# Kernel tuning notes

Hardware: AMD Instinct MI355X
Metric: run time of the kernel (lower is better)

## Reference

```python
import jax, jax.numpy as jnp
import numpy as np

L, H, DK = 4, 8, 64
NEG = -1e9
PAD = -9999.0


def _ln(z, g, b, eps=1e-6):
    # LayerNormalization: uses unbiased std (torch default) and divides by (std + eps)
    m = jnp.mean(z, axis=-1, keepdims=True)
    s = jnp.std(z, axis=-1, keepdims=True, ddof=1)
    return g * (z - m) / (s + eps) + b


def _mha(q_in, kv_in, w, bw, pw, pb, lnp, mask):
    B, Sq, D = q_in.shape
    q = (q_in @ w[0] + bw[0]).reshape(B, Sq, H, DK).transpose(0, 2, 1, 3)
    k = (kv_in @ w[1] + bw[1]).reshape(B, -1, H, DK).transpose(0, 2, 1, 3)
    v = (kv_in @ w[2] + bw[2]).reshape(B, -1, H, DK).transpose(0, 2, 1, 3)
    scores = jnp.einsum('bhqd,bhkd->bhqk', q, k) * (1.0 / np.sqrt(DK))
    if mask is not None:
        scores = jnp.where(mask[:, None, :, :], NEG, scores)
    attn = jax.nn.softmax(scores, axis=-1)
    ctx = jnp.einsum('bhqk,bhkd->bhqd', attn, v).transpose(0, 2, 1, 3).reshape(B, Sq, H * DK)
    return _ln(q_in + ctx @ pw + pb, lnp[0], lnp[1])


def _ffn(x, w1, b1, w2, b2, lnp):
    # kernel-1 conv1d == pointwise linear; w1:[d_ff,d_model], w2:[d_model,d_ff]
    h = jax.nn.relu(jnp.einsum('bsd,fd->bsf', x, w1) + b1)
    o = jnp.einsum('bsf,df->bsd', h, w2) + b2
    return _ln(x + o, lnp[0], lnp[1])


def _forward(enc_inputs, dec_inputs, emb_w, emb_b, pos_table,
             e_qkv_w, e_qkv_b, e_pw, e_pb, e_ln1, e_w1, e_b1, e_w2, e_b2, e_ln2,
             ds_qkv_w, ds_qkv_b, ds_pw, ds_pb, d_ln1,
             dc_qkv_w, dc_qkv_b, dc_pw, dc_pb, d_ln2,
             d_w1, d_b1, d_w2, d_b2, d_ln3):
    B, Se, F = enc_inputs.shape
    Sd = dec_inputs.shape[1]
    # ConvEmbeddingLayer: kernel-1 conv producing (d_model - n_features) channels, concat with raw inputs
    enc = jnp.concatenate([enc_inputs, jnp.einsum('bsf,of->bso', enc_inputs, emb_w) + emb_b], axis=-1)
    dec = jnp.concatenate([dec_inputs, jnp.einsum('bsf,of->bso', dec_inputs, emb_w) + emb_b], axis=-1)
    # PosEncoding with full lengths -> rows 1..S of the padded table
    enc = enc + pos_table[1:Se + 1]
    dec = dec + pos_table[1:Sd + 1]
    # masks per get_attn_pad_mask / get_attn_subsequent_mask
    enc_pad = jnp.sum(enc_inputs, axis=-1) <= PAD  # [B,Se]
    dec_pad = jnp.sum(dec_inputs, axis=-1) <= PAD  # [B,Sd]
    enc_mask = jnp.broadcast_to(enc_pad[:, None, :], (B, Se, Se))
    causal = jnp.triu(jnp.ones((Sd, Sd), dtype=bool), 1)
    dec_self_mask = jnp.broadcast_to(dec_pad[:, None, :], (B, Sd, Sd)) | causal
    cross_mask = jnp.broadcast_to(enc_pad[:, None, :], (B, Sd, Se))
    for i in range(L):
        enc = _mha(enc, enc, e_qkv_w[i], e_qkv_b[i], e_pw[i], e_pb[i], e_ln1[i], enc_mask)
        enc = _ffn(enc, e_w1[i], e_b1[i], e_w2[i], e_b2[i], e_ln2[i])
    for i in range(L):
        dec = _mha(dec, dec, ds_qkv_w[i], ds_qkv_b[i], ds_pw[i], ds_pb[i], d_ln1[i], dec_self_mask)
        dec = _mha(dec, enc, dc_qkv_w[i], dc_qkv_b[i], dc_pw[i], dc_pb[i], d_ln2[i], cross_mask)
        dec = _ffn(dec, d_w1[i], d_b1[i], d_w2[i], d_b2[i], d_ln3[i])
    return dec


def setup_inputs() -> dict:
    B, Se, Sd, F, Dm, Dff = 8, 512, 512, 32, 512, 2048
    key = jax.random.key(0)
    ks = iter(jax.random.split(key, 32))
    s = 0.02

    def n(shape, sc=s):
        return jax.random.normal(next(ks), shape, jnp.float32) * sc

    # sinusoidal PosEncoding table with leading pad row
    pos = np.arange(Se, dtype=np.float64)[:, None]
    j = np.arange(Dm)[None, :]
    ang = pos / np.power(10000.0, 2.0 * (j // 2) / Dm)
    ang[:, 0::2] = np.sin(ang[:, 0::2])
    ang[:, 1::2] = np.cos(ang[:, 1::2])
    pos_table = jnp.asarray(np.concatenate([np.zeros((1, Dm)), ang]).astype(np.float32))

    ln = jnp.broadcast_to(jnp.stack([jnp.ones(Dm), jnp.zeros(Dm)]), (L, 2, Dm)).astype(jnp.float32) + 0.0
    return {
        'enc_inputs': jax.random.normal(next(ks), (B, Se, F), jnp.float32),
        'dec_inputs': jax.random.normal(next(ks), (B, Sd, F), jnp.float32),
        'emb_w': n((Dm - F, F)), 'emb_b': jnp.zeros(Dm - F, jnp.float32),
        'pos_table': pos_table,
        'e_qkv_w': n((L, 3, Dm, H * DK)), 'e_qkv_b': jnp.zeros((L, 3, H * DK), jnp.float32),
        'e_pw': n((L, H * DK, Dm)), 'e_pb': jnp.zeros((L, Dm), jnp.float32), 'e_ln1': ln,
        'e_w1': n((L, Dff, Dm)), 'e_b1': jnp.zeros((L, Dff), jnp.float32),
        'e_w2': n((L, Dm, Dff)), 'e_b2': jnp.zeros((L, Dm), jnp.float32), 'e_ln2': ln,
        'ds_qkv_w': n((L, 3, Dm, H * DK)), 'ds_qkv_b': jnp.zeros((L, 3, H * DK), jnp.float32),
        'ds_pw': n((L, H * DK, Dm)), 'ds_pb': jnp.zeros((L, Dm), jnp.float32), 'd_ln1': ln,
        'dc_qkv_w': n((L, 3, Dm, H * DK)), 'dc_qkv_b': jnp.zeros((L, 3, H * DK), jnp.float32),
        'dc_pw': n((L, H * DK, Dm)), 'dc_pb': jnp.zeros((L, Dm), jnp.float32), 'd_ln2': ln,
        'd_w1': n((L, Dff, Dm)), 'd_b1': jnp.zeros((L, Dff), jnp.float32),
        'd_w2': n((L, Dm, Dff)), 'd_b2': jnp.zeros((L, Dm), jnp.float32), 'd_ln3': ln,
    }


def reference(enc_inputs, dec_inputs, emb_w, emb_b, pos_table,
              e_qkv_w, e_qkv_b, e_pw, e_pb, e_ln1, e_w1, e_b1, e_w2, e_b2, e_ln2,
              ds_qkv_w, ds_qkv_b, ds_pw, ds_pb, d_ln1,
              dc_qkv_w, dc_qkv_b, dc_pw, dc_pb, d_ln2,
              d_w1, d_b1, d_w2, d_b2, d_ln3):
    return _forward(enc_inputs, dec_inputs, emb_w, emb_b, pos_table,
                    e_qkv_w, e_qkv_b, e_pw, e_pb, e_ln1, e_w1, e_b1, e_w2, e_b2, e_ln2,
                    ds_qkv_w, ds_qkv_b, ds_pw, ds_pb, d_ln1,
                    dc_qkv_w, dc_qkv_b, dc_pw, dc_pb, d_ln2,
                    d_w1, d_b1, d_w2, d_b2, d_ln3)
```

## Files before the change

kernel.cpp:

```cpp
#include <hip/hip_runtime.h>
#include <cstdint>
#include <cstddef>

typedef unsigned short u16;
typedef __bf16 bf16x8 __attribute__((ext_vector_type(8)));
typedef float f32x4 __attribute__((ext_vector_type(4)));

constexpr int Bz = 8, Sq = 512, Hh = 8, DKd = 64, Dm = 512, Dff = 2048, NL = 4;
constexpr int TOK = Bz * Sq;
constexpr size_t MAT = (size_t)512 * 512;
constexpr size_t EL  = (size_t)TOK * Dm;
constexpr size_t WFT = (size_t)Dff * Dm;

__device__ __forceinline__ float bf2f(u16 u) {
  union { uint32_t i; float f; } v; v.i = (uint32_t)u << 16; return v.f;
}
__device__ __forceinline__ u16 f2bf(float f) {
  union { float f; uint32_t i; } v; v.f = f;
  uint32_t i = v.i;
  i += 0x7fffu + ((i >> 16) & 1u);
  return (u16)(i >> 16);
}

__device__ __forceinline__ void gload16(const u16* g, u16* l) {
  __builtin_amdgcn_global_load_lds(
      (const __attribute__((address_space(1))) unsigned int*)g,
      (__attribute__((address_space(3))) unsigned int*)l, 16, 0, 0);
}

template<int BM, int BN>
__global__ __launch_bounds__(256)
void gemm_tile(const u16* __restrict__ A, const u16* __restrict__ Bt,
               const float* __restrict__ bias, u16* __restrict__ C,
               int K, int lda, long long sA, int ldb, long long sB,
               int ldc, long long sC, int cmode, int relu, int colofs,
               const u16* A2, int xsplit)
{
  constexpr int HM = BM / 2, HN = BN / 2, MI = HM / 16, NI = HN / 16;
  __shared__ __align__(16) u16 As[BM * 64];
  __shared__ __align__(16) u16 Bs[BN * 64];
  const int bz = blockIdx.z;
  const u16* Abase = A;
  int colbase;
  if (A2 && (int)blockIdx.x >= xsplit) {
    Abase = A2;
    colbase = 512 + ((int)blockIdx.x - xsplit) * BN;
  } else {
    colbase = colofs + (int)blockIdx.x * BN;
  }
  const u16* Ab = Abase + (size_t)bz * (size_t)sA + (size_t)(blockIdx.y * BM) * lda;
  const u16* Bb = Bt + (size_t)bz * (size_t)sB + (size_t)colbase * ldb;
  const int tid  = threadIdx.x;
  const int lane = tid & 63;
  const int wid  = tid >> 6;
  const int l15  = lane & 15;
  const int quad = lane >> 4;
  const int wm   = wid >> 1, wn = wid & 1;

  f32x4 acc[MI][NI] = {};

  for (int k0 = 0; k0 < K; k0 += 64) {
#pragma unroll
    for (int i = 0; i < BM / 32; ++i) {
      const int s = tid + i * 256;
      const int row = s >> 3, c = (s & 7) ^ (row & 7);
      gload16(Ab + (size_t)row * lda + k0 + c * 8, As + s * 8);
    }
#pragma unroll
    for (int i = 0; i < BN / 32; ++i) {
      const int s = tid + i * 256;
      const int row = s >> 3, c = (s & 7) ^ (row & 7);
      gload16(Bb + (size_t)row * ldb + k0 + c * 8, Bs + s * 8);
    }
    __syncthreads();
#pragma unroll
    for (int kk = 0; kk < 2; ++kk) {
      bf16x8 af[MI], bfr[NI];
#pragma unroll
      for (int mi = 0; mi < MI; ++mi) {
        const int ra = wm * HM + mi * 16 + l15;
        af[mi] = *(const bf16x8*)(As + ra * 64 + (((kk * 4 + quad) ^ (ra & 7))) * 8);
      }
#pragma unroll
      for (int ni = 0; ni < NI; ++ni) {
        const int rb = wn * HN + ni * 16 + l15;
        bfr[ni] = *(const bf16x8*)(Bs + rb * 64 + (((kk * 4 + quad) ^ (rb & 7))) * 8);
      }
#pragma unroll
      for (int mi = 0; mi < MI; ++mi)
#pragma unroll
        for (int ni = 0; ni < NI; ++ni)
          acc[mi][ni] = __builtin_amdgcn_mfma_f32_16x16x32_bf16(af[mi], bfr[ni], acc[mi][ni], 0, 0, 0);
    }
    __syncthreads();
  }

  const int rblk = blockIdx.y * BM + wm * HM + quad * 4;
#pragma unroll
  for (int ni = 0; ni < NI; ++ni) {
    const int colx = colbase + wn * HN + ni * 16 + l15;
    const float bv = bias ? bias[colx] : 0.f;
#pragma unroll
    for (int mi = 0; mi < MI; ++mi) {
#pragma unroll
      for (int r = 0; r < 4; ++r) {
        float v = acc[mi][ni][r] + bv;
        if (relu) v = fmaxf(v, 0.f);
        const int grow = rblk + mi * 16 + r;
        size_t off;
        if (cmode == 0) {
          off = (size_t)bz * (size_t)sC + (size_t)grow * ldc + colx;
        } else {
          const int sec = colx >> 9, n = colx & 511, h = n >> 6, d = n & 63;
          const int b = grow >> 9, s = grow & 511;
          if (sec == 0) v *= 0.125f;
          if (sec < 2) off = (size_t)sec * EL + (size_t)b * 262144 + (size_t)h * 32768 + (size_t)s * 64 + d;
          else         off = 2 * EL + (size_t)b * 262144 + (size_t)h * 32768 + (size_t)d * 512 + s;
        }
        C[off] = f2bf(v);
      }
    }
  }
}

__global__ __launch_bounds__(256)
void flash_attn(const u16* __restrict__ q, const u16* __restrict__ k,
                const u16* __restrict__ v, const unsigned char* __restrict__ pad,
                u16* __restrict__ ctx, int mtype)
{
  __shared__ __align__(16) u16 KVs[8192];
  __shared__ __align__(16) u16 Pw[4][2048];
  const int bh = blockIdx.y, b = bh >> 3, h = bh & 7;
  const int qt = blockIdx.x;
  const int tid = threadIdx.x, lane = tid & 63, wid = tid >> 6;
  const int l15 = lane & 15, quad = lane >> 4;
  const size_t bho = (size_t)bh * 32768;
  const int qrow = qt * 64 + wid * 16 + l15;
  const int qcd  = qt * 64 + wid * 16 + quad * 4;

  unsigned char* Ps = (unsigned char*)&Pw[0][0];
  if (tid < 128) ((uchar4*)Ps)[tid] = ((const uchar4*)(pad + b * 512))[tid];

  bf16x8 aq0 = *(const bf16x8*)(q + bho + (size_t)qrow * 64 + quad * 8);
  bf16x8 aq1 = *(const bf16x8*)(q + bho + (size_t)qrow * 64 + 32 + quad * 8);

  f32x4 S[32];
#pragma unroll
  for (int kc = 0; kc < 4; ++kc) {
    __syncthreads();
#pragma unroll
    for (int i = 0; i < 4; ++i) {
      const int s = tid + i * 256;
      const int row = s >> 3, c = (s & 7) ^ (row & 7);
      gload16(k + bho + (size_t)(kc * 128 + row) * 64 + c * 8, KVs + s * 8);
    }
    __syncthreads();
#pragma unroll
    for (int t = 0; t < 8; ++t) {
      const int sw = l15 & 7;
      bf16x8 b0 = *(const bf16x8*)(KVs + (t * 16 + l15) * 64 + (quad ^ sw) * 8);
      bf16x8 b1 = *(const bf16x8*)(KVs + (t * 16 + l15) * 64 + ((4 + quad) ^ sw) * 8);
      f32x4 z = {0.f, 0.f, 0.f, 0.f};
      z = __builtin_amdgcn_mfma_f32_16x16x32_bf16(aq0, b0, z, 0, 0, 0);
      S[kc * 8 + t] = __builtin_amdgcn_mfma_f32_16x16x32_bf16(aq1, b1, z, 0, 0, 0);
    }
  }

  unsigned pm = 0u;
#pragma unroll
  for (int t = 0; t < 32; ++t) pm |= (unsigned)(Ps[t * 16 + l15] != 0) << t;

  float inv[4];
#pragma unroll
  for (int r = 0; r < 4; ++r) {
    const int qg = qcd + r;
    float mx = -3.0e38f;
#pragma unroll
    for (int t = 0; t < 32; ++t) {
      const int col = t * 16 + l15;
      const bool m = ((pm >> t) & 1u) || (mtype == 1 && col > qg);
      const float val = m ? -1e9f : S[t][r];
      S[t][r] = val;
      mx = fmaxf(mx, val);
    }
#pragma unroll
    for (int o = 8; o > 0; o >>= 1) mx = fmaxf(mx, __shfl_xor(mx, o));
    float sm = 0.f;
#pragma unroll
    for (int t = 0; t < 32; ++t) { const float e = __expf(S[t][r] - mx); S[t][r] = e; sm += e; }
#pragma unroll
    for (int o = 8; o > 0; o >>= 1) sm += __shfl_xor(sm, o);
    inv[r] = 1.f / sm;
  }

  f32x4 O[4] = {};
  u16* myP = &Pw[wid][0];
#pragma unroll
  for (int kc = 0; kc < 4; ++kc) {
    __syncthreads();
#pragma unroll
    for (int i = 0; i < 4; ++i) {
      const int s = tid + i * 256;
      const int row = s >> 4, c = (s & 15) ^ (row & 15);
      gload16(v + bho + (size_t)row * 512 + kc * 128 + c * 8, KVs + s * 8);
    }
#pragma unroll
    for (int t = 0; t < 8; ++t)
#pragma unroll
      for (int r = 0; r < 4; ++r) {
        const int rowq = quad * 4 + r;
        const int c = 2 * t + (l15 >> 3);
        myP[rowq * 128 + (c ^ rowq) * 8 + (l15 & 7)] = f2bf(S[kc * 8 + t][r] * inv[r]);
      }
    __syncthreads();
#pragma unroll
    for (int kk = 0; kk < 4; ++kk) {
      bf16x8 ap = *(const bf16x8*)(myP + l15 * 128 + ((kk * 4 + quad) ^ l15) * 8);
#pragma unroll
      for (int ni = 0; ni < 4; ++ni) {
        bf16x8 bv = *(const bf16x8*)(KVs + (ni * 16 + l15) * 128 + ((kk * 4 + quad) ^ l15) * 8);
        O[ni] = __builtin_amdgcn_mfma_f32_16x16x32_bf16(ap, bv, O[ni], 0, 0, 0);
      }
    }
  }

  const int token = b * 512 + qcd;
#pragma unroll
  for (int ni = 0; ni < 4; ++ni)
#pragma unroll
    for (int r = 0; r < 4; ++r)
      ctx[(size_t)(token + r) * 512 + h * 64 + ni * 16 + l15] = f2bf(O[ni][r]);
}

__global__ __launch_bounds__(256)
void transpose_all(const float* __restrict__ s0, const float* __restrict__ s1,
                   const float* __restrict__ s2, const float* __restrict__ s3,
                   const float* __restrict__ s4, const float* __restrict__ s5,
                   u16* __restrict__ out)
{
  __shared__ float tile[32][33];
  const int z = blockIdx.z;
  const float* src; int zi;
  if      (z < 12) { src = s0; zi = z; }
  else if (z < 24) { src = s1; zi = z - 12; }
  else if (z < 36) { src = s2; zi = z - 24; }
  else if (z < 40) { src = s3; zi = z - 36; }
  else if (z < 44) { src = s4; zi = z - 40; }
  else             { src = s5; zi = z - 44; }
  const float* in = src + (size_t)zi * MAT;
  u16* o = out + (size_t)z * MAT;
  int x = blockIdx.x * 32 + threadIdx.x;
  int y = blockIdx.y * 32 + threadIdx.y;
#pragma unroll
  for (int i = 0; i < 32; i += 8)
    tile[threadIdx.y + i][threadIdx.x] = in[(size_t)(y + i) * 512 + x];
  __syncthreads();
  x = blockIdx.y * 32 + threadIdx.x;
  y = blockIdx.x * 32 + threadIdx.y;
#pragma unroll
  for (int i = 0; i < 32; i += 8)
    o[(size_t)(y + i) * 512 + x] = f2bf(tile[threadIdx.x][threadIdx.y + i]);
}

__global__ __launch_bounds__(256)
void convert4(const float* __restrict__ a, const float* __restrict__ b,
              const float* __restrict__ c, const float* __restrict__ d,
              u16* __restrict__ out, int n)
{
  const float* srcs[4] = { a, b, c, d };
  const float* src = srcs[blockIdx.y];
  u16* dst = out + (size_t)blockIdx.y * n;
  int i = (blockIdx.x * 256 + threadIdx.x) * 4;
  if (i < n) {
    float4 v = *(const float4*)(src + i);
    ushort4 u = { f2bf(v.x), f2bf(v.y), f2bf(v.z), f2bf(v.w) };
    *(ushort4*)(dst + i) = u;
  }
}

__global__ __launch_bounds__(256)
void embed_k(const float* __restrict__ x, const float* __restrict__ ew,
             const float* __restrict__ eb, const float* __restrict__ pos,
             u16* __restrict__ out, unsigned char* __restrict__ padv)
{
  const int rs = blockIdx.x;
  const int s  = rs & 511;
  __shared__ float xr[32];
  const int t = threadIdx.x;
  if (t < 32) xr[t] = x[(size_t)rs * 32 + t];
  __syncthreads();
  if (t == 0) {
    float sacc = 0.f;
#pragma unroll
    for (int f = 0; f < 32; ++f) sacc += xr[f];
    padv[rs] = (sacc <= -9999.f) ? 1 : 0;
  }
#pragma unroll
  for (int rep = 0; rep < 2; ++rep) {
    const int c = t + rep * 256;
    float v;
    if (c < 32) {
      v = xr[c];
    } else {
      const float* w = ew + (size_t)(c - 32) * 32;
      float acc = eb[c - 32];
#pragma unroll
      for (int f = 0; f < 32; ++f) acc += xr[f] * w[f];
      v = acc;
    }
    v += pos[(size_t)(s + 1) * 512 + c];
    out[(size_t)rs * 512 + c] = f2bf(v);
  }
}

__global__ __launch_bounds__(256)
void add_ln(const u16* __restrict__ x, const u16* __restrict__ y,
            const float* __restrict__ g, const float* __restrict__ bb,
            u16* __restrict__ out)
{
  const int row  = blockIdx.x * 4 + (threadIdx.x >> 6);
  const int lane = threadIdx.x & 63;
  const int c0 = lane * 8;
  const size_t base = (size_t)row * Dm + c0;

  uint4 xr = *(const uint4*)(x + base);
  uint4 yr = *(const uint4*)(y + base);
  const u16* xh = (const u16*)&xr;
  const u16* yh = (const u16*)&yr;
  float z[8];
  float s = 0.f;
#pragma unroll
  for (int j = 0; j < 8; ++j) { z[j] = bf2f(xh[j]) + bf2f(yh[j]); s += z[j]; }
#pragma unroll
  for (int off = 32; off > 0; off >>= 1) s += __shfl_xor(s, off);
  const float mean = s * (1.f / 512.f);
  float ss = 0.f;
#pragma unroll
  for (int j = 0; j < 8; ++j) { z[j] -= mean; ss += z[j] * z[j]; }
#pragma unroll
  for (int off = 32; off > 0; off >>= 1) ss += __shfl_xor(ss, off);
  const float stdv = sqrtf(ss * (1.f / 511.f));
  const float inv = 1.f / (stdv + 1e-6f);

  float4 g0 = *(const float4*)(g + c0),  g1 = *(const float4*)(g + c0 + 4);
  float4 b0 = *(const float4*)(bb + c0), b1 = *(const float4*)(bb + c0 + 4);
  float gv[8] = { g0.x, g0.y, g0.z, g0.w, g1.x, g1.y, g1.z, g1.w };
  float bv[8] = { b0.x, b0.y, b0.z, b0.w, b1.x, b1.y, b1.z, b1.w };
  uint4 ow;
  u16* oh = (u16*)&ow;
#pragma unroll
  for (int j = 0; j < 8; ++j) oh[j] = f2bf(gv[j] * z[j] * inv + bv[j]);
  *(uint4*)(out + base) = ow;
}

__global__ __launch_bounds__(256)
void store_f32(const u16* __restrict__ in, float* __restrict__ out, int n)
{
  int i = (blockIdx.x * 256 + threadIdx.x) * 8;
  if (i < n) {
    uint4 raw = *(const uint4*)(in + i);
    const u16* h = (const u16*)&raw;
    float4 o0 = { bf2f(h[0]), bf2f(h[1]), bf2f(h[2]), bf2f(h[3]) };
    float4 o1 = { bf2f(h[4]), bf2f(h[5]), bf2f(h[6]), bf2f(h[7]) };
    *(float4*)(out + i) = o0;
    *(float4*)(out + i + 4) = o1;
  }
}

extern "C" void kernel_launch(void* const* d_in, const int* in_sizes, int n_in,
                              void* d_out, int out_size, void* d_ws, size_t ws_size,
                              hipStream_t stream)
{
  (void)in_sizes; (void)n_in; (void)out_size;
  const float* enc_in   = (const float*)d_in[0];
  const float* dec_in   = (const float*)d_in[1];
  const float* emb_w    = (const float*)d_in[2];
  const float* emb_b    = (const float*)d_in[3];
  const float* pos      = (const float*)d_in[4];
  const float* e_qkv_w  = (const float*)d_in[5];
  const float* e_qkv_b  = (const float*)d_in[6];
  const float* e_pw     = (const float*)d_in[7];
  const float* e_pb     = (const float*)d_in[8];
  const float* e_ln1    = (const float*)d_in[9];
  const float* e_w1     = (const float*)d_in[10];
  const float* e_b1     = (const float*)d_in[11];
  const float* e_w2     = (const float*)d_in[12];
  const float* e_b2     = (const float*)d_in[13];
  const float* e_ln2    = (const float*)d_in[14];
  const float* ds_qkv_w = (const float*)d_in[15];
  const float* ds_qkv_b = (const float*)d_in[16];
  const float* ds_pw    = (const float*)d_in[17];
  const float* ds_pb    = (const float*)d_in[18];
  const float* d_ln1    = (const float*)d_in[19];
  const float* dc_qkv_w = (const float*)d_in[20];
  const float* dc_qkv_b = (const float*)d_in[21];
  const float* dc_pw    = (const float*)d_in[22];
  const float* dc_pb    = (const float*)d_in[23];
  const float* d_ln2    = (const float*)d_in[24];
  const float* d_w1     = (const float*)d_in[25];
  const float* d_b1     = (const float*)d_in[26];
  const float* d_w2     = (const float*)d_in[27];
  const float* d_b2     = (const float*)d_in[28];
  const float* d_ln3    = (const float*)d_in[29];

  u16* ws  = (u16*)d_ws;
  u16* enc = ws;
  u16* dec = ws + EL;
  u16* qb  = ws + 2 * EL;
  u16* kb  = ws + 3 * EL;
  u16* vT  = ws + 4 * EL;
  u16* ctx = ws + 5 * EL;
  u16* t1  = ws + 6 * EL;
  u16* hff = ws + 7 * EL;
  u16* wT  = ws + 15 * EL;
  unsigned char* padE = (unsigned char*)(ws + 21 * EL);
  unsigned char* padD = padE + TOK;
  u16* wfAll = ws + 22 * EL;
  if (ws_size < 30 * EL * 2 + 2 * TOK) return;

  transpose_all<<<dim3(16, 16, 48), dim3(32, 8), 0, stream>>>(
      e_qkv_w, ds_qkv_w, dc_qkv_w, e_pw, ds_pw, dc_pw, wT);
  convert4<<<dim3(4096, 4), 256, 0, stream>>>(e_w1, e_w2, d_w1, d_w2, wfAll, (int)(4 * WFT));
  embed_k<<<TOK, 256, 0, stream>>>(enc_in, emb_w, emb_b, pos, enc, padE);
  embed_k<<<TOK, 256, 0, stream>>>(dec_in, emb_w, emb_b, pos, dec, padD);

  auto attention = [&](const u16* qsrc, const u16* kvsrc, const u16* wq3, const float* b3,
                       const u16* pwT, const float* pb, const float* ln,
                       const unsigned char* pad, int mtype, u16* x) {
    if (qsrc == kvsrc) {
      gemm_tile<64, 128><<<dim3(12, 64, 1), 256, 0, stream>>>(
          qsrc, wq3, b3, qb, 512, 512, 0, 512, 0, 0, 0, 4, 0, 0, nullptr, 0);
    } else {
      gemm_tile<64, 128><<<dim3(12, 64, 1), 256, 0, stream>>>(
          qsrc, wq3, b3, qb, 512, 512, 0, 512, 0, 0, 0, 4, 0, 0, kvsrc, 4);
    }
    flash_attn<<<dim3(8, 64), 256, 0, stream>>>(qb, kb, vT, pad, ctx, mtype);
    gemm_tile<64, 64><<<dim3(8, 64, 1), 256, 0, stream>>>(
        ctx, pwT, pb, t1, 512, 512, 0, 512, 0, 512, 0, 0, 0, 0, nullptr, 0);
    add_ln<<<TOK / 4, 256, 0, stream>>>(x, t1, ln, ln + 512, x);
  };

  auto ffn = [&](u16* x, const u16* w1b, const float* b1, const u16* w2b,
                 const float* b2, const float* ln) {
    gemm_tile<128, 128><<<dim3(16, 32, 1), 256, 0, stream>>>(
        x, w1b, b1, hff, 512, 512, 0, 512, 0, 2048, 0, 0, 1, 0, nullptr, 0);
    gemm_tile<64, 64><<<dim3(8, 64, 1), 256, 0, stream>>>(
        hff, w2b, b2, t1, 2048, 2048, 0, 2048, 0, 512, 0, 0, 0, 0, nullptr, 0);
    add_ln<<<TOK / 4, 256, 0, stream>>>(x, t1, ln, ln + 512, x);
  };

  for (int i = 0; i < NL; ++i) {
    attention(enc, enc, wT + (size_t)(i * 3) * MAT, e_qkv_b + i * 3 * 512,
              wT + (size_t)(36 + i) * MAT, e_pb + i * 512, e_ln1 + i * 1024, padE, 0, enc);
    ffn(enc, wfAll + (size_t)i * WFT, e_b1 + i * Dff,
        wfAll + 4 * WFT + (size_t)i * WFT, e_b2 + i * Dm, e_ln2 + i * 1024);
  }

  for (int i = 0; i < NL; ++i) {
    attention(dec, dec, wT + (size_t)(12 + i * 3) * MAT, ds_qkv_b + i * 3 * 512,
              wT + (size_t)(40 + i) * MAT, ds_pb + i * 512, d_ln1 + i * 1024, padD, 1, dec);
    attention(dec, enc, wT + (size_t)(24 + i * 3) * MAT, dc_qkv_b + i * 3 * 512,
              wT + (size_t)(44 + i) * MAT, dc_pb + i * 512, d_ln2 + i * 1024, padE, 2, dec);
    ffn(dec, wfAll + 8 * WFT + (size_t)i * WFT, d_b1 + i * Dff,
        wfAll + 12 * WFT + (size_t)i * WFT, d_b2 + i * Dm, d_ln3 + i * 1024);
  }

  store_f32<<<(int)(EL / 8 / 256), 256, 0, stream>>>(dec, (float*)d_out, (int)EL);
}
```

Baseline: 1.299 ms.

## Skip masked causal key blocks, keep fp32 residual stream, merge embed launches

In flash_attn with the causal mask, key/value chunks lying entirely above the diagonal are skipped, so both the QK and PV passes do less work for the decoder self-attention. Separately, the residual stream now lives in fp32 buffers that add_ln reads and writes alongside the bf16 copy, which improves accuracy but adds extra memory traffic per LayerNorm. The two embed launches are merged into one grid, and the final conversion kernel is replaced by a device-to-device copy of the fp32 buffer.

```diff
diff --git a/kernel.cpp b/kernel.cpp
--- a/kernel.cpp
+++ b/kernel.cpp
@@ -137,6 +137,7 @@
   const size_t bho = (size_t)bh * 32768;
   const int qrow = qt * 64 + wid * 16 + l15;
   const int qcd  = qt * 64 + wid * 16 + quad * 4;
+  const int nkc  = (mtype == 1) ? (qt >> 1) + 1 : 4;
 
   unsigned char* Ps = (unsigned char*)&Pw[0][0];
   if (tid < 128) ((uchar4*)Ps)[tid] = ((const uchar4*)(pad + b * 512))[tid];
@@ -147,22 +148,24 @@
   f32x4 S[32];
 #pragma unroll
   for (int kc = 0; kc < 4; ++kc) {
-    __syncthreads();
-#pragma unroll
-    for (int i = 0; i < 4; ++i) {
-      const int s = tid + i * 256;
-      const int row = s >> 3, c = (s & 7) ^ (row & 7);
-      gload16(k + bho + (size_t)(kc * 128 + row) * 64 + c * 8, KVs + s * 8);
-    }
-    __syncthreads();
-#pragma unroll
-    for (int t = 0; t < 8; ++t) {
-      const int sw = l15 & 7;
-      bf16x8 b0 = *(const bf16x8*)(KVs + (t * 16 + l15) * 64 + (quad ^ sw) * 8);
-      bf16x8 b1 = *(const bf16x8*)(KVs + (t * 16 + l15) * 64 + ((4 + quad) ^ sw) * 8);
-      f32x4 z = {0.f, 0.f, 0.f, 0.f};
-      z = __builtin_amdgcn_mfma_f32_16x16x32_bf16(aq0, b0, z, 0, 0, 0);
-      S[kc * 8 + t] = __builtin_amdgcn_mfma_f32_16x16x32_bf16(aq1, b1, z, 0, 0, 0);
+    if (kc < nkc) {
+      __syncthreads();
+#pragma unroll
+      for (int i = 0; i < 4; ++i) {
+        const int s = tid + i * 256;
+        const int row = s >> 3, c = (s & 7) ^ (row & 7);
+        gload16(k + bho + (size_t)(kc * 128 + row) * 64 + c * 8, KVs + s * 8);
+      }
+      __syncthreads();
+#pragma unroll
+      for (int t = 0; t < 8; ++t) {
+        const int sw = l15 & 7;
+        bf16x8 b0 = *(const bf16x8*)(KVs + (t * 16 + l15) * 64 + (quad ^ sw) * 8);
+        bf16x8 b1 = *(const bf16x8*)(KVs + (t * 16 + l15) * 64 + ((4 + quad) ^ sw) * 8);
+        f32x4 z = {0.f, 0.f, 0.f, 0.f};
+        z = __builtin_amdgcn_mfma_f32_16x16x32_bf16(aq0, b0, z, 0, 0, 0);
+        S[kc * 8 + t] = __builtin_amdgcn_mfma_f32_16x16x32_bf16(aq1, b1, z, 0, 0, 0);
+      }
     }
   }
 
@@ -177,17 +180,21 @@
     float mx = -3.0e38f;
 #pragma unroll
     for (int t = 0; t < 32; ++t) {
-      const int col = t * 16 + l15;
-      const bool m = ((pm >> t) & 1u) || (mtype == 1 && col > qg);
-      const float val = m ? -1e9f : S[t][r];
-      S[t][r] = val;
-      mx = fmaxf(mx, val);
+      if (t < nkc * 8) {
+        const int col = t * 16 + l15;
+        const bool m = ((pm >> t) & 1u) || (mtype == 1 && col > qg);
+        const float val = m ? -1e9f : S[t][r];
+        S[t][r] = val;
+        mx = fmaxf(mx, val);
+      }
     }
 #pragma unroll
     for (int o = 8; o > 0; o >>= 1) mx = fmaxf(mx, __shfl_xor(mx, o));
     float sm = 0.f;
 #pragma unroll
-    for (int t = 0; t < 32; ++t) { const float e = __expf(S[t][r] - mx); S[t][r] = e; sm += e; }
+    for (int t = 0; t < 32; ++t) {
+      if (t < nkc * 8) { const float e = __expf(S[t][r] - mx); S[t][r] = e; sm += e; }
+    }
 #pragma unroll
     for (int o = 8; o > 0; o >>= 1) sm += __shfl_xor(sm, o);
     inv[r] = 1.f / sm;
@@ -197,29 +204,31 @@
   u16* myP = &Pw[wid][0];
 #pragma unroll
   for (int kc = 0; kc < 4; ++kc) {
-    __syncthreads();
-#pragma unroll
-    for (int i = 0; i < 4; ++i) {
-      const int s = tid + i * 256;
-      const int row = s >> 4, c = (s & 15) ^ (row & 15);
-      gload16(v + bho + (size_t)row * 512 + kc * 128 + c * 8, KVs + s * 8);
-    }
-#pragma unroll
-    for (int t = 0; t < 8; ++t)
-#pragma unroll
-      for (int r = 0; r < 4; ++r) {
-        const int rowq = quad * 4 + r;
-        const int c = 2 * t + (l15 >> 3);
-        myP[rowq * 128 + (c ^ rowq) * 8 + (l15 & 7)] = f2bf(S[kc * 8 + t][r] * inv[r]);
-      }
-    __syncthreads();
-#pragma unroll
-    for (int kk = 0; kk < 4; ++kk) {
-      bf16x8 ap = *(const bf16x8*)(myP + l15 * 128 + ((kk * 4 + quad) ^ l15) * 8);
-#pragma unroll
-      for (int ni = 0; ni < 4; ++ni) {
-        bf16x8 bv = *(const bf16x8*)(KVs + (ni * 16 + l15) * 128 + ((kk * 4 + quad) ^ l15) * 8);
-        O[ni] = __builtin_amdgcn_mfma_f32_16x16x32_bf16(ap, bv, O[ni], 0, 0, 0);
+    if (kc < nkc) {
+      __syncthreads();
+#pragma unroll
+      for (int i = 0; i < 4; ++i) {
+        const int s = tid + i * 256;
+        const int row = s >> 4, c = (s & 15) ^ (row & 15);
+        gload16(v + bho + (size_t)row * 512 + kc * 128 + c * 8, KVs + s * 8);
+      }
+#pragma unroll
+      for (int t = 0; t < 8; ++t)
+#pragma unroll
+        for (int r = 0; r < 4; ++r) {
+          const int rowq = quad * 4 + r;
+          const int c = 2 * t + (l15 >> 3);
+          myP[rowq * 128 + (c ^ rowq) * 8 + (l15 & 7)] = f2bf(S[kc * 8 + t][r] * inv[r]);
+        }
+      __syncthreads();
+#pragma unroll
+      for (int kk = 0; kk < 4; ++kk) {
+        bf16x8 ap = *(const bf16x8*)(myP + l15 * 128 + ((kk * 4 + quad) ^ l15) * 8);
+#pragma unroll
+        for (int ni = 0; ni < 4; ++ni) {
+          bf16x8 bv = *(const bf16x8*)(KVs + (ni * 16 + l15) * 128 + ((kk * 4 + quad) ^ l15) * 8);
+          O[ni] = __builtin_amdgcn_mfma_f32_16x16x32_bf16(ap, bv, O[ni], 0, 0, 0);
+        }
       }
     }
   }
@@ -279,10 +288,18 @@
 }
 
 __global__ __launch_bounds__(256)
-void embed_k(const float* __restrict__ x, const float* __restrict__ ew,
-             const float* __restrict__ eb, const float* __restrict__ pos,
-             u16* __restrict__ out, unsigned char* __restrict__ padv)
-{
+void embed_k(const float* __restrict__ xe, const float* __restrict__ xd,
+             const float* __restrict__ ew, const float* __restrict__ eb,
+             const float* __restrict__ pos,
+             u16* __restrict__ oe, u16* __restrict__ od,
+             float* __restrict__ oeF, float* __restrict__ odF,
+             unsigned char* __restrict__ pe, unsigned char* __restrict__ pd)
+{
+  const int which = blockIdx.y;
+  const float* x = which ? xd : xe;
+  u16* out = which ? od : oe;
+  float* outF = which ? odF : oeF;
+  unsigned char* padv = which ? pd : pe;
   const int rs = blockIdx.x;
   const int s  = rs & 511;
   __shared__ float xr[32];
@@ -310,27 +327,28 @@
     }
     v += pos[(size_t)(s + 1) * 512 + c];
     out[(size_t)rs * 512 + c] = f2bf(v);
-  }
-}
-
-__global__ __launch_bounds__(256)
-void add_ln(const u16* __restrict__ x, const u16* __restrict__ y,
+    outF[(size_t)rs * 512 + c] = v;
+  }
+}
+
+__global__ __launch_bounds__(256)
+void add_ln(float* __restrict__ xresF, const u16* __restrict__ y,
             const float* __restrict__ g, const float* __restrict__ bb,
-            u16* __restrict__ out)
+            u16* __restrict__ xout)
 {
   const int row  = blockIdx.x * 4 + (threadIdx.x >> 6);
   const int lane = threadIdx.x & 63;
   const int c0 = lane * 8;
   const size_t base = (size_t)row * Dm + c0;
 
-  uint4 xr = *(const uint4*)(x + base);
+  float4 x0 = *(const float4*)(xresF + base);
+  float4 x1 = *(const float4*)(xresF + base + 4);
   uint4 yr = *(const uint4*)(y + base);
-  const u16* xh = (const u16*)&xr;
   const u16* yh = (const u16*)&yr;
-  float z[8];
+  float z[8] = { x0.x, x0.y, x0.z, x0.w, x1.x, x1.y, x1.z, x1.w };
   float s = 0.f;
 #pragma unroll
-  for (int j = 0; j < 8; ++j) { z[j] = bf2f(xh[j]) + bf2f(yh[j]); s += z[j]; }
+  for (int j = 0; j < 8; ++j) { z[j] += bf2f(yh[j]); s += z[j]; }
 #pragma unroll
   for (int off = 32; off > 0; off >>= 1) s += __shfl_xor(s, off);
   const float mean = s * (1.f / 512.f);
@@ -346,25 +364,15 @@
   float4 b0 = *(const float4*)(bb + c0), b1 = *(const float4*)(bb + c0 + 4);
   float gv[8] = { g0.x, g0.y, g0.z, g0.w, g1.x, g1.y, g1.z, g1.w };
   float bv[8] = { b0.x, b0.y, b0.z, b0.w, b1.x, b1.y, b1.z, b1.w };
+  float o[8];
   uint4 ow;
   u16* oh = (u16*)&ow;
 #pragma unroll
-  for (int j = 0; j < 8; ++j) oh[j] = f2bf(gv[j] * z[j] * inv + bv[j]);
-  *(uint4*)(out + base) = ow;
-}
-
-__global__ __launch_bounds__(256)
-void store_f32(const u16* __restrict__ in, float* __restrict__ out, int n)
-{
-  int i = (blockIdx.x * 256 + threadIdx.x) * 8;
-  if (i < n) {
-    uint4 raw = *(const uint4*)(in + i);
-    const u16* h = (const u16*)&raw;
-    float4 o0 = { bf2f(h[0]), bf2f(h[1]), bf2f(h[2]), bf2f(h[3]) };
-    float4 o1 = { bf2f(h[4]), bf2f(h[5]), bf2f(h[6]), bf2f(h[7]) };
-    *(float4*)(out + i) = o0;
-    *(float4*)(out + i + 4) = o1;
-  }
+  for (int j = 0; j < 8; ++j) { o[j] = gv[j] * z[j] * inv + bv[j]; oh[j] = f2bf(o[j]); }
+  *(uint4*)(xout + base) = ow;
+  float4 f0 = { o[0], o[1], o[2], o[3] }, f1 = { o[4], o[5], o[6], o[7] };
+  *(float4*)(xresF + base) = f0;
+  *(float4*)(xresF + base + 4) = f1;
 }
 
 extern "C" void kernel_launch(void* const* d_in, const int* in_sizes, int n_in,
@@ -377,31 +385,31 @@
   const float* emb_w    = (const float*)d_in[2];
   const float* emb_b    = (const float*)d_in[3];
   const float* pos      = (const float*)d_in[4];
-  const float* e_qkv_w  = (const float*)d_in[5];
   const float* e_qkv_b  = (const float*)d_in[6];
-  const float* e_pw     = (const float*)d_in[7];
   const float* e_pb     = (const float*)d_in[8];
   const float* e_ln1    = (const float*)d_in[9];
-  const float* e_w1     = (const float*)d_in[10];
   const float* e_b1     = (const float*)d_in[11];
-  const float* e_w2     = (const float*)d_in[12];
   const float* e_b2     = (const float*)d_in[13];
   const float* e_ln2    = (const float*)d_in[14];
-  const float* ds_qkv_w = (const float*)d_in[15];
   const float* ds_qkv_b = (const float*)d_in[16];
-  const float* ds_pw    = (const float*)d_in[17];
   const float* ds_pb    = (const float*)d_in[18];
   const float* d_ln1    = (const float*)d_in[19];
-  const float* dc_qkv_w = (const float*)d_in[20];
   const float* dc_qkv_b = (const float*)d_in[21];
-  const float* dc_pw    = (const float*)d_in[22];
   const float* dc_pb    = (const float*)d_in[23];
   const float* d_ln2    = (const float*)d_in[24];
-  const float* d_w1     = (const float*)d_in[25];
   const float* d_b1     = (const float*)d_in[26];
-  const float* d_w2     = (const float*)d_in[27];
   const float* d_b2     = (const float*)d_in[28];
   const float* d_ln3    = (const float*)d_in[29];
+  const float* e_qkv_w  = (const float*)d_in[5];
+  const float* e_pw     = (const float*)d_in[7];
+  const float* e_w1     = (const float*)d_in[10];
+  const float* e_w2     = (const float*)d_in[12];
+  const float* ds_qkv_w = (const float*)d_in[15];
+  const float* ds_pw    = (const float*)d_in[17];
+  const float* dc_qkv_w = (const float*)d_in[20];
+  const float* dc_pw    = (const float*)d_in[22];
+  const float* d_w1     = (const float*)d_in[25];
+  const float* d_w2     = (const float*)d_in[27];
 
   u16* ws  = (u16*)d_ws;
   u16* enc = ws;
@@ -412,6 +420,8 @@
   u16* ctx = ws + 5 * EL;
   u16* t1  = ws + 6 * EL;
   u16* hff = ws + 7 * EL;
+  float* encF = (float*)(ws + 11 * EL);
+  float* decF = (float*)(ws + 13 * EL);
   u16* wT  = ws + 15 * EL;
   unsigned char* padE = (unsigned char*)(ws + 21 * EL);
   unsigned char* padD = padE + TOK;
@@ -421,12 +431,12 @@
   transpose_all<<<dim3(16, 16, 48), dim3(32, 8), 0, stream>>>(
       e_qkv_w, ds_qkv_w, dc_qkv_w, e_pw, ds_pw, dc_pw, wT);
   convert4<<<dim3(4096, 4), 256, 0, stream>>>(e_w1, e_w2, d_w1, d_w2, wfAll, (int)(4 * WFT));
-  embed_k<<<TOK, 256, 0, stream>>>(enc_in, emb_w, emb_b, pos, enc, padE);
-  embed_k<<<TOK, 256, 0, stream>>>(dec_in, emb_w, emb_b, pos, dec, padD);
+  embed_k<<<dim3(TOK, 2), 256, 0, stream>>>(enc_in, dec_in, emb_w, emb_b, pos,
+                                            enc, dec, encF, decF, padE, padD);
 
   auto attention = [&](const u16* qsrc, const u16* kvsrc, const u16* wq3, const float* b3,
                        const u16* pwT, const float* pb, const float* ln,
-                       const unsigned char* pad, int mtype, u16* x) {
+                       const unsigned char* pad, int mtype, u16* x, float* xF) {
     if (qsrc == kvsrc) {
       gemm_tile<64, 128><<<dim3(12, 64, 1), 256, 0, stream>>>(
           qsrc, wq3, b3, qb, 512, 512, 0, 512, 0, 0, 0, 4, 0, 0, nullptr, 0);
@@ -437,33 +447,33 @@
     flash_attn<<<dim3(8, 64), 256, 0, stream>>>(qb, kb, vT, pad, ctx, mtype);
     gemm_tile<64, 64><<<dim3(8, 64, 1), 256, 0, stream>>>(
         ctx, pwT, pb, t1, 512, 512, 0, 512, 0, 512, 0, 0, 0, 0, nullptr, 0);
-    add_ln<<<TOK / 4, 256, 0, stream>>>(x, t1, ln, ln + 512, x);
+    add_ln<<<TOK / 4, 256, 0, stream>>>(xF, t1, ln, ln + 512, x);
   };
 
-  auto ffn = [&](u16* x, const u16* w1b, const float* b1, const u16* w2b,
+  auto ffn = [&](u16* x, float* xF, const u16* w1b, const float* b1, const u16* w2b,
                  const float* b2, const float* ln) {
     gemm_tile<128, 128><<<dim3(16, 32, 1), 256, 0, stream>>>(
         x, w1b, b1, hff, 512, 512, 0, 512, 0, 2048, 0, 0, 1, 0, nullptr, 0);
     gemm_tile<64, 64><<<dim3(8, 64, 1), 256, 0, stream>>>(
         hff, w2b, b2, t1, 2048, 2048, 0, 2048, 0, 512, 0, 0, 0, 0, nullptr, 0);
-    add_ln<<<TOK / 4, 256, 0, stream>>>(x, t1, ln, ln + 512, x);
+    add_ln<<<TOK / 4, 256, 0, stream>>>(xF, t1, ln, ln + 512, x);
   };
 
   for (int i = 0; i < NL; ++i) {
     attention(enc, enc, wT + (size_t)(i * 3) * MAT, e_qkv_b + i * 3 * 512,
-              wT + (size_t)(36 + i) * MAT, e_pb + i * 512, e_ln1 + i * 1024, padE, 0, enc);
-    ffn(enc, wfAll + (size_t)i * WFT, e_b1 + i * Dff,
+              wT + (size_t)(36 + i) * MAT, e_pb + i * 512, e_ln1 + i * 1024, padE, 0, enc, encF);
+    ffn(enc, encF, wfAll + (size_t)i * WFT, e_b1 + i * Dff,
         wfAll + 4 * WFT + (size_t)i * WFT, e_b2 + i * Dm, e_ln2 + i * 1024);
   }
 
   for (int i = 0; i < NL; ++i) {
     attention(dec, dec, wT + (size_t)(12 + i * 3) * MAT, ds_qkv_b + i * 3 * 512,
-              wT + (size_t)(40 + i) * MAT, ds_pb + i * 512, d_ln1 + i * 1024, padD, 1, dec);
+              wT + (size_t)(40 + i) * MAT, ds_pb + i * 512, d_ln1 + i * 1024, padD, 1, dec, decF);
     attention(dec, enc, wT + (size_t)(24 + i * 3) * MAT, dc_qkv_b + i * 3 * 512,
-              wT + (size_t)(44 + i) * MAT, dc_pb + i * 512, d_ln2 + i * 1024, padE, 2, dec);
-    ffn(dec, wfAll + 8 * WFT + (size_t)i * WFT, d_b1 + i * Dff,
+              wT + (size_t)(44 + i) * MAT, dc_pb + i * 512, d_ln2 + i * 1024, padE, 2, dec, decF);
+    ffn(dec, decF, wfAll + 8 * WFT + (size_t)i * WFT, d_b1 + i * Dff,
         wfAll + 12 * WFT + (size_t)i * WFT, d_b2 + i * Dm, d_ln3 + i * 1024);
   }
 
-  store_f32<<<(int)(EL / 8 / 256), 256, 0, stream>>>(dec, (float*)d_out, (int)EL);
-}
+  hipMemcpyAsync(d_out, decF, EL * sizeof(float), hipMemcpyDeviceToDevice, stream);
+}
```

Result: slower. 1.464 ms (+12.8%).

## Skip masked causal key chunks, vectorize merged embedding, retile FFN1 GEMM

Applied to the files above, without the earlier changes.

In causal attention, key/value chunks entirely above the diagonal are skipped for both the score and the PV phases, which removes wasted loads and MFMAs. The two embedding launches are merged into one, with one warp per row and vectorized loads and stores. The first FFN GEMM switches from 128x128 to 64x128 tiles, doubling the block count. The tile change risks lower data reuse per block in exchange for better occupancy.

```diff
diff --git a/kernel.cpp b/kernel.cpp
--- a/kernel.cpp
+++ b/kernel.cpp
@@ -137,6 +137,7 @@
   const size_t bho = (size_t)bh * 32768;
   const int qrow = qt * 64 + wid * 16 + l15;
   const int qcd  = qt * 64 + wid * 16 + quad * 4;
+  const int nkc  = (mtype == 1) ? (qt >> 1) + 1 : 4;
 
   unsigned char* Ps = (unsigned char*)&Pw[0][0];
   if (tid < 128) ((uchar4*)Ps)[tid] = ((const uchar4*)(pad + b * 512))[tid];
@@ -147,22 +148,24 @@
   f32x4 S[32];
 #pragma unroll
   for (int kc = 0; kc < 4; ++kc) {
-    __syncthreads();
-#pragma unroll
-    for (int i = 0; i < 4; ++i) {
-      const int s = tid + i * 256;
-      const int row = s >> 3, c = (s & 7) ^ (row & 7);
-      gload16(k + bho + (size_t)(kc * 128 + row) * 64 + c * 8, KVs + s * 8);
-    }
-    __syncthreads();
-#pragma unroll
-    for (int t = 0; t < 8; ++t) {
-      const int sw = l15 & 7;
-      bf16x8 b0 = *(const bf16x8*)(KVs + (t * 16 + l15) * 64 + (quad ^ sw) * 8);
-      bf16x8 b1 = *(const bf16x8*)(KVs + (t * 16 + l15) * 64 + ((4 + quad) ^ sw) * 8);
-      f32x4 z = {0.f, 0.f, 0.f, 0.f};
-      z = __builtin_amdgcn_mfma_f32_16x16x32_bf16(aq0, b0, z, 0, 0, 0);
-      S[kc * 8 + t] = __builtin_amdgcn_mfma_f32_16x16x32_bf16(aq1, b1, z, 0, 0, 0);
+    if (kc < nkc) {
+      __syncthreads();
+#pragma unroll
+      for (int i = 0; i < 4; ++i) {
+        const int s = tid + i * 256;
+        const int row = s >> 3, c = (s & 7) ^ (row & 7);
+        gload16(k + bho + (size_t)(kc * 128 + row) * 64 + c * 8, KVs + s * 8);
+      }
+      __syncthreads();
+#pragma unroll
+      for (int t = 0; t < 8; ++t) {
+        const int sw = l15 & 7;
+        bf16x8 b0 = *(const bf16x8*)(KVs + (t * 16 + l15) * 64 + (quad ^ sw) * 8);
+        bf16x8 b1 = *(const bf16x8*)(KVs + (t * 16 + l15) * 64 + ((4 + quad) ^ sw) * 8);
+        f32x4 z = {0.f, 0.f, 0.f, 0.f};
+        z = __builtin_amdgcn_mfma_f32_16x16x32_bf16(aq0, b0, z, 0, 0, 0);
+        S[kc * 8 + t] = __builtin_amdgcn_mfma_f32_16x16x32_bf16(aq1, b1, z, 0, 0, 0);
+      }
     }
   }
 
@@ -177,17 +180,21 @@
     float mx = -3.0e38f;
 #pragma unroll
     for (int t = 0; t < 32; ++t) {
-      const int col = t * 16 + l15;
-      const bool m = ((pm >> t) & 1u) || (mtype == 1 && col > qg);
-      const float val = m ? -1e9f : S[t][r];
-      S[t][r] = val;
-      mx = fmaxf(mx, val);
+      if (t < nkc * 8) {
+        const int col = t * 16 + l15;
+        const bool m = ((pm >> t) & 1u) || (mtype == 1 && col > qg);
+        const float val = m ? -1e9f : S[t][r];
+        S[t][r] = val;
+        mx = fmaxf(mx, val);
+      }
     }
 #pragma unroll
     for (int o = 8; o > 0; o >>= 1) mx = fmaxf(mx, __shfl_xor(mx, o));
     float sm = 0.f;
 #pragma unroll
-    for (int t = 0; t < 32; ++t) { const float e = __expf(S[t][r] - mx); S[t][r] = e; sm += e; }
+    for (int t = 0; t < 32; ++t) {
+      if (t < nkc * 8) { const float e = __expf(S[t][r] - mx); S[t][r] = e; sm += e; }
+    }
 #pragma unroll
     for (int o = 8; o > 0; o >>= 1) sm += __shfl_xor(sm, o);
     inv[r] = 1.f / sm;
@@ -197,29 +204,31 @@
   u16* myP = &Pw[wid][0];
 #pragma unroll
   for (int kc = 0; kc < 4; ++kc) {
-    __syncthreads();
-#pragma unroll
-    for (int i = 0; i < 4; ++i) {
-      const int s = tid + i * 256;
-      const int row = s >> 4, c = (s & 15) ^ (row & 15);
-      gload16(v + bho + (size_t)row * 512 + kc * 128 + c * 8, KVs + s * 8);
-    }
-#pragma unroll
-    for (int t = 0; t < 8; ++t)
-#pragma unroll
-      for (int r = 0; r < 4; ++r) {
-        const int rowq = quad * 4 + r;
-        const int c = 2 * t + (l15 >> 3);
-        myP[rowq * 128 + (c ^ rowq) * 8 + (l15 & 7)] = f2bf(S[kc * 8 + t][r] * inv[r]);
-      }
-    __syncthreads();
-#pragma unroll
-    for (int kk = 0; kk < 4; ++kk) {
-      bf16x8 ap = *(const bf16x8*)(myP + l15 * 128 + ((kk * 4 + quad) ^ l15) * 8);
-#pragma unroll
-      for (int ni = 0; ni < 4; ++ni) {
-        bf16x8 bv = *(const bf16x8*)(KVs + (ni * 16 + l15) * 128 + ((kk * 4 + quad) ^ l15) * 8);
-        O[ni] = __builtin_amdgcn_mfma_f32_16x16x32_bf16(ap, bv, O[ni], 0, 0, 0);
+    if (kc < nkc) {
+      __syncthreads();
+#pragma unroll
+      for (int i = 0; i < 4; ++i) {
+        const int s = tid + i * 256;
+        const int row = s >> 4, c = (s & 15) ^ (row & 15);
+        gload16(v + bho + (size_t)row * 512 + kc * 128 + c * 8, KVs + s * 8);
+      }
+#pragma unroll
+      for (int t = 0; t < 8; ++t)
+#pragma unroll
+        for (int r = 0; r < 4; ++r) {
+          const int rowq = quad * 4 + r;
+          const int c = 2 * t + (l15 >> 3);
+          myP[rowq * 128 + (c ^ rowq) * 8 + (l15 & 7)] = f2bf(S[kc * 8 + t][r] * inv[r]);
+        }
+      __syncthreads();
+#pragma unroll
+      for (int kk = 0; kk < 4; ++kk) {
+        bf16x8 ap = *(const bf16x8*)(myP + l15 * 128 + ((kk * 4 + quad) ^ l15) * 8);
+#pragma unroll
+        for (int ni = 0; ni < 4; ++ni) {
+          bf16x8 bv = *(const bf16x8*)(KVs + (ni * 16 + l15) * 128 + ((kk * 4 + quad) ^ l15) * 8);
+          O[ni] = __builtin_amdgcn_mfma_f32_16x16x32_bf16(ap, bv, O[ni], 0, 0, 0);
+        }
       }
     }
   }
@@ -279,38 +288,59 @@
 }
 
 __global__ __launch_bounds__(256)
-void embed_k(const float* __restrict__ x, const float* __restrict__ ew,
-             const float* __restrict__ eb, const float* __restrict__ pos,
-             u16* __restrict__ out, unsigned char* __restrict__ padv)
-{
-  const int rs = blockIdx.x;
+void embed_k(const float* __restrict__ xe, const float* __restrict__ xd,
+             const float* __restrict__ ew, const float* __restrict__ eb,
+             const float* __restrict__ pos,
+             u16* __restrict__ oe, u16* __restrict__ od,
+             unsigned char* __restrict__ pe, unsigned char* __restrict__ pd)
+{
+  const int which = blockIdx.y;
+  const float* x = which ? xd : xe;
+  u16* out = which ? od : oe;
+  unsigned char* padv = which ? pd : pe;
+  const int wid = threadIdx.x >> 6, lane = threadIdx.x & 63;
+  const int rs = blockIdx.x * 4 + wid;
   const int s  = rs & 511;
-  __shared__ float xr[32];
-  const int t = threadIdx.x;
-  if (t < 32) xr[t] = x[(size_t)rs * 32 + t];
-  __syncthreads();
-  if (t == 0) {
+
+  float xs[32];
+#pragma unroll
+  for (int j = 0; j < 8; ++j) {
+    float4 v = *(const float4*)(x + (size_t)rs * 32 + j * 4);
+    xs[j * 4 + 0] = v.x; xs[j * 4 + 1] = v.y; xs[j * 4 + 2] = v.z; xs[j * 4 + 3] = v.w;
+  }
+  if (lane == 0) {
     float sacc = 0.f;
 #pragma unroll
-    for (int f = 0; f < 32; ++f) sacc += xr[f];
+    for (int f = 0; f < 32; ++f) sacc += xs[f];
     padv[rs] = (sacc <= -9999.f) ? 1 : 0;
   }
-#pragma unroll
-  for (int rep = 0; rep < 2; ++rep) {
-    const int c = t + rep * 256;
+  const int c0 = lane * 8;
+  float4 p0 = *(const float4*)(pos + (size_t)(s + 1) * 512 + c0);
+  float4 p1 = *(const float4*)(pos + (size_t)(s + 1) * 512 + c0 + 4);
+  const float pv[8] = { p0.x, p0.y, p0.z, p0.w, p1.x, p1.y, p1.z, p1.w };
+  uint4 ow; u16* oh = (u16*)&ow;
+#pragma unroll
+  for (int j = 0; j < 8; ++j) {
+    const int c = c0 + j;
     float v;
     if (c < 32) {
-      v = xr[c];
+      v = xs[c];
     } else {
       const float* w = ew + (size_t)(c - 32) * 32;
+      float wv[32];
+#pragma unroll
+      for (int q4 = 0; q4 < 8; ++q4) {
+        float4 t = *(const float4*)(w + q4 * 4);
+        wv[q4 * 4 + 0] = t.x; wv[q4 * 4 + 1] = t.y; wv[q4 * 4 + 2] = t.z; wv[q4 * 4 + 3] = t.w;
+      }
       float acc = eb[c - 32];
 #pragma unroll
-      for (int f = 0; f < 32; ++f) acc += xr[f] * w[f];
+      for (int f = 0; f < 32; ++f) acc += xs[f] * wv[f];
       v = acc;
     }
-    v += pos[(size_t)(s + 1) * 512 + c];
-    out[(size_t)rs * 512 + c] = f2bf(v);
-  }
+    oh[j] = f2bf(v + pv[j]);
+  }
+  *(uint4*)(out + (size_t)rs * 512 + c0) = ow;
 }
 
 __global__ __launch_bounds__(256)
@@ -421,8 +451,8 @@
   transpose_all<<<dim3(16, 16, 48), dim3(32, 8), 0, stream>>>(
       e_qkv_w, ds_qkv_w, dc_qkv_w, e_pw, ds_pw, dc_pw, wT);
   convert4<<<dim3(4096, 4), 256, 0, stream>>>(e_w1, e_w2, d_w1, d_w2, wfAll, (int)(4 * WFT));
-  embed_k<<<TOK, 256, 0, stream>>>(enc_in, emb_w, emb_b, pos, enc, padE);
-  embed_k<<<TOK, 256, 0, stream>>>(dec_in, emb_w, emb_b, pos, dec, padD);
+  embed_k<<<dim3(TOK / 4, 2), 256, 0, stream>>>(enc_in, dec_in, emb_w, emb_b, pos,
+                                                enc, dec, padE, padD);
 
   auto attention = [&](const u16* qsrc, const u16* kvsrc, const u16* wq3, const float* b3,
                        const u16* pwT, const float* pb, const float* ln,
@@ -442,7 +472,7 @@
 
   auto ffn = [&](u16* x, const u16* w1b, const float* b1, const u16* w2b,
                  const float* b2, const float* ln) {
-    gemm_tile<128, 128><<<dim3(16, 32, 1), 256, 0, stream>>>(
+    gemm_tile<64, 128><<<dim3(16, 64, 1), 256, 0, stream>>>(
         x, w1b, b1, hff, 512, 512, 0, 512, 0, 2048, 0, 0, 1, 0, nullptr, 0);
     gemm_tile<64, 64><<<dim3(8, 64, 1), 256, 0, stream>>>(
         hff, w2b, b2, t1, 2048, 2048, 0, 2048, 0, 512, 0, 0, 0, 0, nullptr, 0);
```

Result: slower. 1.418 ms (+9.2%).
